# Kernel tuning notes

Measured on AMD Instinct MI355X. Metric: run time of the kernel, lower is better.

## Reference

```python
import jax, jax.numpy as jnp
import numpy as np

B, N, C, H, W = 16, 8, 3, 48, 48
K = 5          # kernel_size=[5]
NK = 4         # hardcoded multi-kernel weight groups in the module


def setup_inputs() -> dict:
    key = jax.random.key(0)
    k1, k2, k3 = jax.random.split(key, 3)
    frames = jax.random.normal(k1, (B, N, C, H, W), jnp.float32)
    # core as produced by _convert_dict: [B, N, K*K, 3, 4, H, W]
    core = jax.random.normal(k2, (B, N, K * K, C, NK, H, W), jnp.float32)
    kernel_weight = jax.random.normal(k3, (B, N, NK, C, H, W), jnp.float32)
    return {"frames": frames, "core": core, "kernel_weight": kernel_weight}


def reference(frames, core, kernel_weight):
    b, n, c, h, w = frames.shape
    kk = K * K
    # torch: padded_kernel = stack([core[5]], dim=2) -> [B,N,1,25,3,4,H,W]
    #        .view(B, N, 4, -1, 3, 48, 48): row-major reinterpretation of the
    #        flattened (25*3*4)=300 middle dims into (4, 25, 3).
    pk = core.reshape(b, n, NK, kk, c, h, w)
    # kernel_weight.unsqueeze(3) -> [B,N,4,1,3,H,W]; mean over the 4 groups
    wk = jnp.mean(pk * kernel_weight[:, :, :, None], axis=2)  # [B,N,25,3,H,W]
    # im2col-style gather: pad by K//2 and stack the 25 spatial shifts
    p = K // 2
    fp = jnp.pad(frames, ((0, 0), (0, 0), (0, 0), (p, p), (p, p)))
    img_stack = jnp.stack(
        [fp[..., i:i + h, j:j + w] for i in range(K) for j in range(K)],
        axis=2,
    )  # [B,N,25,3,H,W]
    # pred_rgb[i] = sum_k sum_c wk[:,:,k,i] * img_stack[:,:,k,c]
    frames_sum = jnp.sum(img_stack, axis=3)  # [B,N,25,H,W]
    pred_img_i = jnp.einsum('bnkihw,bnkhw->bnihw', wk, frames_sum)  # [B,N,3,H,W]
    pred_img = jnp.mean(pred_img_i, axis=1)  # [B,3,H,W]
    return pred_img_i, pred_img
```

## Files before the change

### kernel.cpp

```cpp
#include <hip/hip_runtime.h>
#include <stdint.h>
#include <stddef.h>

constexpr int B_ = 16, N_ = 8, C_ = 3, H_ = 48, W_ = 48, K_ = 5, NK_ = 4;
constexpr int HW_ = H_ * W_;
constexpr int IMGS_ = B_ * N_;
constexpr int PW_ = W_ + 4;
constexpr int PH_ = H_ + 4;
constexpr int PHW_ = PH_ * PW_;
constexpr int HWH_ = HW_ / 2;

__global__ void kcs(const float* __restrict__ frames, float* __restrict__ cs) {
    int id = blockIdx.x * blockDim.x + threadIdx.x;
    if (id >= IMGS_ * PHW_) return;
    int img = id / PHW_;
    int rem = id - img * PHW_;
    int ph = rem / PW_;
    int pw = rem - ph * PW_;
    int h = ph - 2, w = pw - 2;
    float s = 0.f;
    if ((unsigned)h < (unsigned)H_ && (unsigned)w < (unsigned)W_) {
        const float* f = frames + (size_t)img * (C_ * HW_) + h * W_ + w;
        s = f[0] + f[HW_] + f[2 * HW_];
    }
    cs[id] = s;
}

__global__ __launch_bounds__(64) void kmain(const float* __restrict__ core,
                                            const float* __restrict__ kw,
                                            const float* __restrict__ cs,
                                            float* __restrict__ out) {
    int tid = blockIdx.x * 64 + threadIdx.x;
    int img = tid / HWH_;
    int r = tid - img * HWH_;
    int h = r / (W_ / 2);
    int wg = r - h * (W_ / 2);
    int w0 = wg * 2;
    int pix0 = h * W_ + w0;

    float fs[5][6];
    const float* csp = cs + img * PHW_ + h * PW_ + w0;
#pragma unroll
    for (int rr = 0; rr < 5; ++rr) {
        const float2* rp = (const float2*)(csp + rr * PW_);
        float2 a = rp[0], b = rp[1], c = rp[2];
        fs[rr][0] = a.x; fs[rr][1] = a.y;
        fs[rr][2] = b.x; fs[rr][3] = b.y;
        fs[rr][4] = c.x; fs[rr][5] = c.y;
    }

    const float* cp = core + (size_t)img * (300 * HW_) + pix0;
    const float* kp = kw + (size_t)img * (12 * HW_) + pix0;

    float p0[3] = {0.f, 0.f, 0.f};
    float p1[3] = {0.f, 0.f, 0.f};
    for (int g = 0; g < 4; ++g) {
#pragma unroll
        for (int c = 0; c < 3; ++c) {
            float t0 = 0.f, t1 = 0.f;
            const float* cpk = cp + (size_t)(g * 75 + c) * HW_;
#pragma unroll
            for (int k = 0; k < 25; ++k) {
                float2 d = *(const float2*)(cpk + (size_t)(k * 3) * HW_);
                int di = k / 5, dj = k - di * 5;
                t0 += d.x * fs[di][dj];
                t1 += d.y * fs[di][dj + 1];
            }
            float2 kd = *(const float2*)(kp + (size_t)(g * 3 + c) * HW_);
            p0[c] += kd.x * t0;
            p1[c] += kd.y * t1;
        }
    }

    float* op = out + (size_t)img * (3 * HW_) + pix0;
#pragma unroll
    for (int c = 0; c < 3; ++c) {
        float2 v = make_float2(0.25f * p0[c], 0.25f * p1[c]);
        *(float2*)(op + (size_t)c * HW_) = v;
    }
}

__global__ void kmean(const float* __restrict__ outi, float* __restrict__ outm) {
    int id = blockIdx.x * blockDim.x + threadIdx.x;
    if (id >= B_ * 3 * HW_) return;
    int b = id / (3 * HW_);
    int rem = id - b * (3 * HW_);
    const float* p = outi + (size_t)b * (N_ * 3 * HW_) + rem;
    float s = 0.f;
#pragma unroll
    for (int n = 0; n < N_; ++n) s += p[(size_t)n * 3 * HW_];
    outm[id] = s * 0.125f;
}

extern "C" void kernel_launch(void* const* d_in, const int* in_sizes, int n_in,
                              void* d_out, int out_size, void* d_ws, size_t ws_size,
                              hipStream_t stream) {
    const float* frames = (const float*)d_in[0];
    const float* core = (const float*)d_in[1];
    const float* kw = (const float*)d_in[2];
    float* cs = (float*)d_ws;
    float* outi = (float*)d_out;
    float* outm = outi + (size_t)B_ * N_ * 3 * HW_;

    kcs<<<(IMGS_ * PHW_ + 255) / 256, 256, 0, stream>>>(frames, cs);
    kmain<<<IMGS_ * HWH_ / 64, 64, 0, stream>>>(core, kw, cs, outi);
    kmean<<<(B_ * 3 * HW_ + 255) / 256, 256, 0, stream>>>(outi, outm);
}
```

Baseline: 482.6 us.

## Split main kernel into per-group/row-segment partial sums plus combine pass

Replaces the per-pixel-pair main kernel with a kernel where each block handles one image, one weight group and one kernel row (5 taps × 3 channels). It computes 4 pixels per lane with 128-bit loads and writes partial sums to a workspace. A second kernel reduces the 20 partials per image and channel and applies kernel_weight and the 1/4 factor. The goal is more parallelism and wider, coalesced loads over the large core tensor. The cost is an extra kernel launch and a partial buffer about 20× the output size that must be written and read back.

```diff
diff --git a/kernel.cpp b/kernel.cpp
--- a/kernel.cpp
+++ b/kernel.cpp
@@ -8,7 +8,8 @@
 constexpr int PW_ = W_ + 4;
 constexpr int PH_ = H_ + 4;
 constexpr int PHW_ = PH_ * PW_;
-constexpr int HWH_ = HW_ / 2;
+
+typedef float f32x4 __attribute__((ext_vector_type(4)));
 
 __global__ void kcs(const float* __restrict__ frames, float* __restrict__ cs) {
     int id = blockIdx.x * blockDim.x + threadIdx.x;
@@ -26,58 +27,95 @@
     cs[id] = s;
 }
 
-__global__ __launch_bounds__(64) void kmain(const float* __restrict__ core,
-                                            const float* __restrict__ kw,
-                                            const float* __restrict__ cs,
-                                            float* __restrict__ out) {
-    int tid = blockIdx.x * 64 + threadIdx.x;
-    int img = tid / HWH_;
-    int r = tid - img * HWH_;
-    int h = r / (W_ / 2);
-    int wg = r - h * (W_ / 2);
-    int w0 = wg * 2;
-    int pix0 = h * W_ + w0;
+__global__ __launch_bounds__(192) void kpart(const float* __restrict__ core,
+                                             const float* __restrict__ cs,
+                                             float* __restrict__ partial) {
+    int b = blockIdx.x;
+    int img = b / 20;
+    int r = b - img * 20;
+    int g = r / 5;
+    int seg = r - g * 5;
+    int t = threadIdx.x;
 
-    float fs[5][6];
-    const float* csp = cs + img * PHW_ + h * PW_ + w0;
+    int q0 = t, q1 = t + 192, q2 = t + 384;
+    int h0 = q0 / 12, w00 = (q0 % 12) * 4;
+    int h1 = q1 / 12, w01 = (q1 % 12) * 4;
+    int h2 = q2 / 12, w02 = (q2 % 12) * 4;
+
+    float fs[3][8];
+    {
+        const float* ci = cs + (size_t)img * PHW_;
+        const float* r0 = ci + (h0 + seg) * PW_ + w00;
+        const float* r1 = ci + (h1 + seg) * PW_ + w01;
+        const float* r2 = ci + (h2 + seg) * PW_ + w02;
+        f32x4 a0 = *(const f32x4*)r0, b0 = *(const f32x4*)(r0 + 4);
+        f32x4 a1 = *(const f32x4*)r1, b1 = *(const f32x4*)(r1 + 4);
+        f32x4 a2 = *(const f32x4*)r2, b2 = *(const f32x4*)(r2 + 4);
 #pragma unroll
-    for (int rr = 0; rr < 5; ++rr) {
-        const float2* rp = (const float2*)(csp + rr * PW_);
-        float2 a = rp[0], b = rp[1], c = rp[2];
-        fs[rr][0] = a.x; fs[rr][1] = a.y;
-        fs[rr][2] = b.x; fs[rr][3] = b.y;
-        fs[rr][4] = c.x; fs[rr][5] = c.y;
-    }
-
-    const float* cp = core + (size_t)img * (300 * HW_) + pix0;
-    const float* kp = kw + (size_t)img * (12 * HW_) + pix0;
-
-    float p0[3] = {0.f, 0.f, 0.f};
-    float p1[3] = {0.f, 0.f, 0.f};
-    for (int g = 0; g < 4; ++g) {
-#pragma unroll
-        for (int c = 0; c < 3; ++c) {
-            float t0 = 0.f, t1 = 0.f;
-            const float* cpk = cp + (size_t)(g * 75 + c) * HW_;
-#pragma unroll
-            for (int k = 0; k < 25; ++k) {
-                float2 d = *(const float2*)(cpk + (size_t)(k * 3) * HW_);
-                int di = k / 5, dj = k - di * 5;
-                t0 += d.x * fs[di][dj];
-                t1 += d.y * fs[di][dj + 1];
-            }
-            float2 kd = *(const float2*)(kp + (size_t)(g * 3 + c) * HW_);
-            p0[c] += kd.x * t0;
-            p1[c] += kd.y * t1;
+        for (int j = 0; j < 4; ++j) {
+            fs[0][j] = a0[j]; fs[0][j + 4] = b0[j];
+            fs[1][j] = a1[j]; fs[1][j + 4] = b1[j];
+            fs[2][j] = a2[j]; fs[2][j + 4] = b2[j];
         }
     }
 
-    float* op = out + (size_t)img * (3 * HW_) + pix0;
+    const float* cb = core + ((size_t)img * 300 + g * 75 + seg * 15) * HW_;
+
+    f32x4 acc[3][3] = {};
+#pragma unroll
+    for (int k5 = 0; k5 < 5; ++k5) {
+#pragma unroll
+        for (int c = 0; c < 3; ++c) {
+            const float* pp = cb + (size_t)(k5 * 3 + c) * HW_;
+            f32x4 d0 = *(const f32x4*)(pp + q0 * 4);
+            f32x4 d1 = *(const f32x4*)(pp + q1 * 4);
+            f32x4 d2 = *(const f32x4*)(pp + q2 * 4);
+#pragma unroll
+            for (int j = 0; j < 4; ++j) {
+                acc[c][0][j] += d0[j] * fs[0][k5 + j];
+                acc[c][1][j] += d1[j] * fs[1][k5 + j];
+                acc[c][2][j] += d2[j] * fs[2][k5 + j];
+            }
+        }
+    }
+
+    float* pb = partial + (((size_t)img * 4 + g) * 5 + seg) * (3 * HW_);
 #pragma unroll
     for (int c = 0; c < 3; ++c) {
-        float2 v = make_float2(0.25f * p0[c], 0.25f * p1[c]);
-        *(float2*)(op + (size_t)c * HW_) = v;
+        *(f32x4*)(pb + (size_t)c * HW_ + q0 * 4) = acc[c][0];
+        *(f32x4*)(pb + (size_t)c * HW_ + q1 * 4) = acc[c][1];
+        *(f32x4*)(pb + (size_t)c * HW_ + q2 * 4) = acc[c][2];
     }
+}
+
+__global__ void kcomb(const float* __restrict__ partial,
+                      const float* __restrict__ kw,
+                      float* __restrict__ outi) {
+    int id = blockIdx.x * blockDim.x + threadIdx.x;
+    int img = id / (3 * (HW_ / 4));
+    int r = id - img * (3 * (HW_ / 4));
+    int c = r / (HW_ / 4);
+    int q = r - c * (HW_ / 4);
+    int p = q * 4;
+
+    f32x4 o = {0.f, 0.f, 0.f, 0.f};
+#pragma unroll
+    for (int g = 0; g < 4; ++g) {
+        f32x4 s = {0.f, 0.f, 0.f, 0.f};
+#pragma unroll
+        for (int seg = 0; seg < 5; ++seg) {
+            f32x4 v = *(const f32x4*)(partial +
+                (((size_t)img * 4 + g) * 5 + seg) * (3 * HW_) + (size_t)c * HW_ + p);
+#pragma unroll
+            for (int j = 0; j < 4; ++j) s[j] += v[j];
+        }
+        f32x4 kd = *(const f32x4*)(kw + ((size_t)img * 12 + g * 3 + c) * HW_ + p);
+#pragma unroll
+        for (int j = 0; j < 4; ++j) o[j] += kd[j] * s[j];
+    }
+#pragma unroll
+    for (int j = 0; j < 4; ++j) o[j] *= 0.25f;
+    *(f32x4*)(outi + ((size_t)img * 3 + c) * HW_ + p) = o;
 }
 
 __global__ void kmean(const float* __restrict__ outi, float* __restrict__ outm) {
@@ -99,10 +137,12 @@
     const float* core = (const float*)d_in[1];
     const float* kw = (const float*)d_in[2];
     float* cs = (float*)d_ws;
+    float* partial = cs + (size_t)IMGS_ * PHW_;
     float* outi = (float*)d_out;
     float* outm = outi + (size_t)B_ * N_ * 3 * HW_;
 
     kcs<<<(IMGS_ * PHW_ + 255) / 256, 256, 0, stream>>>(frames, cs);
-    kmain<<<IMGS_ * HWH_ / 64, 64, 0, stream>>>(core, kw, cs, outi);
+    kpart<<<IMGS_ * NK_ * 5, 192, 0, stream>>>(core, cs, partial);
+    kcomb<<<(IMGS_ * 3 * (HW_ / 4)) / 256, 256, 0, stream>>>(partial, kw, outi);
     kmean<<<(B_ * 3 * HW_ + 255) / 256, 256, 0, stream>>>(outi, outm);
 }
```

New measurement: 501.1 us. 3.8% more time.
